# Kernel tuning notes

Hardware: AMD Instinct MI355X
Metric: run time of the kernel (lower is better)

Reference implementation:

```python
import jax, jax.numpy as jnp
import numpy as np

N, B, PG, L, HC, EC, H, NC, KNN = 256, 4, 64, 32, 128, 64, 4, 14, 8
D = HC // H
CUTOFF = 10.0
LOG2 = 0.6931471805599453

_counts = np.array([14, 5, 11, 8, 8, 6, 9, 9, 4, 10, 8, 8, 9, 8, 11, 7, 6, 7, 14, 12, 7])
RES_ATOM_MASK = (np.arange(14)[None, :] < _counts[:, None]).astype(np.float32)  # [21,14]


def _ln(x, g, b):
    mu = jnp.mean(x, -1, keepdims=True)
    var = jnp.mean((x - mu) ** 2, -1, keepdims=True)
    return (x - mu) / jnp.sqrt(var + 1e-5) * g + b


def _ssp(x):
    return jax.nn.softplus(x) - LOG2


def _safe_norm(x):
    return jnp.sqrt(jnp.maximum(jnp.sum(x * x, -1), 1e-12))


def _seg_softmax(x, idx, n):
    m = jax.ops.segment_max(x, idx, num_segments=n)
    e = jnp.exp(x - m[idx])
    s = jax.ops.segment_sum(e, idx, num_segments=n)
    return e / s[idx]


def _smear(d):
    offs = jnp.linspace(0.0, CUTOFF, EC)
    coeff = -0.5 / (offs[1] - offs[0]) ** 2
    return jnp.exp(coeff * (d[..., None] - offs) ** 2)


def _core(res_H, res_X, ligand_pos, ligand_feat, ligand_mask,
          ln_g, ln_b, ln1_g, ln1_b,
          WQ, WK, WV, WKl, WVl, WO, WOl, WOl1,
          Ti_w1, Ti_b1, Ti_w2, Ti_b2,
          sD_w1, sD_b1, sD_w2, sD_b2,
          sD1_w1, sD1_b1, sD1_w2, sD1_b2,
          res_S, batch, residue_mask, row1, col1):
    n = res_H.shape[0]
    bsz = ligand_feat.shape[0]
    lc = ligand_feat.shape[1]
    amask = jnp.asarray(RES_ATOM_MASK)[res_S]  # [n,14]

    # kNN graph on C-alpha (atom 1), per-graph, flow target_to_source, + self loops
    ctr = res_X[:, 1]
    d2 = jnp.sum((ctr[:, None] - ctr[None]) ** 2, -1)
    bad = (batch[:, None] != batch[None]) | jnp.eye(n, dtype=bool)
    _, nbr = jax.lax.top_k(-jnp.where(bad, jnp.inf, d2), KNN)
    row = jnp.concatenate([jnp.repeat(jnp.arange(n), KNN), jnp.arange(n)])
    col = jnp.concatenate([nbr.reshape(-1), jnp.arange(n)])

    Rij = _safe_norm(res_X[row][:, :, None] - res_X[col][:, None])  # [E,14,14]
    drep = _smear(Rij)  # [E,14,14,EC]

    res_Hn = _ln(res_H, ln_g, ln_b)
    Q = (res_Hn @ WQ.T).reshape(n, NC, H, D)
    Kt = (res_Hn @ WK.T).reshape(n, NC, H, D)
    V = (res_Hn @ WV.T).reshape(n, NC, H, D)

    logits = jnp.einsum('ephd,eqhd->ehpq', Q[row], Kt[col]) / np.sqrt(D)
    sig = jax.nn.relu(drep @ sD_w1.T + sD_b1) @ sD_w2.T + sD_b2  # [E,14,14,H]
    logits = logits + sig.transpose(0, 3, 1, 2)

    am_e = amask[row][:, :, None] * amask[col][:, None]  # [E,14,14]
    r = jnp.einsum('ep,ehpq,eq->eh', amask[row], logits, amask[col])
    r = r / jnp.sum(am_e, (-1, -2))[:, None]
    beta = _seg_softmax(r, row, n)  # [E,H]

    att = jax.nn.softmax(logits, -1) * am_e[:, None]
    att = att / (jnp.sum(jnp.abs(att), -1, keepdims=True) + 1e-7)
    aV = jnp.einsum('ehpq,eqhd->ehpd', att, V[col])
    updH = jax.ops.segment_sum(beta[:, :, None, None] * aV, row, num_segments=n)
    updH = updH.transpose(0, 2, 1, 3).reshape(n, NC, HC)
    res_H2 = (res_Hn + _ssp(updH) @ WO.T) * amask[..., None]

    Xij = res_X[row][:, :, None] - res_X[col][:, None]  # [E,14,14,3]
    Xij = Xij / (_safe_norm(Xij)[..., None] + 1e-5)
    Qf = Q.reshape(n, NC, HC)
    Kf = Kt.reshape(n, NC, HC)
    # T_i on concat([Q_p, K_q, dist]) computed as split matmuls (no big concat)
    hmid = (Qf[row] @ Ti_w1[:, :HC].T)[:, :, None, :] \
        + (Kf[col] @ Ti_w1[:, HC:2 * HC].T)[:, None, :, :] \
        + drep @ Ti_w1[:, 2 * HC:].T + Ti_b1  # [E,14,14,HC]
    f = (jax.nn.relu(hmid) @ Ti_w2.T + Ti_b2)[..., 0]  # [E,14,14]
    f = f * jnp.mean(att, 1)
    dX = jax.ops.segment_sum(jnp.mean(beta, -1)[:, None, None]
                             * jnp.sum(f[..., None] * Xij, -2), row, num_segments=n)
    res_X2 = jnp.where(residue_mask[:, None, None],
                       res_X + jnp.clip(dX, -3.0, 3.0), res_X)

    # residue <-> ligand cross attention over (editable residue, graph) edges
    lf = _ln(ligand_feat, ln1_g, ln1_b)
    Kl = (lf @ WKl.T).reshape(bsz, lc, H, D)
    Vl = (lf @ WVl.T).reshape(bsz, lc, H, D)
    Rij1 = _safe_norm(res_X2[row1][:, :, None] - ligand_pos[col1][:, None])
    drep1 = _smear(Rij1)  # [E1,14,L,EC]
    lg = jnp.einsum('ephd,eqhd->ehpq', Q[row1], Kl[col1]) / np.sqrt(D)
    sig1 = jax.nn.relu(drep1 @ sD1_w1.T + sD1_b1) @ sD1_w2.T + sD1_b2
    lg = lg + sig1.transpose(0, 3, 1, 2)

    am1 = amask[row1][:, :, None] * ligand_mask[col1][:, None]  # [E1,14,L]
    r1 = jnp.einsum('ep,ehpq,eq->eh', amask[row1], lg, ligand_mask[col1])
    r1 = r1 / jnp.sum(am1, (-1, -2))[:, None]
    beta1 = _seg_softmax(r1, col1, bsz)

    ar = jax.nn.softmax(lg, -1) * am1[:, None]
    ar = ar / (jnp.sum(jnp.abs(ar), -1, keepdims=True) + 1e-7)
    al = jax.nn.softmax(lg, -2) * am1[:, None]
    # faithful to source: lig branch divided by L1 norm of already-normalized ar
    al = al / (jnp.sum(jnp.abs(ar), -1, keepdims=True) + 1e-7)
    aVr = jnp.einsum('ehpq,eqhd->ehpd', ar, Vl[col1])  # [E1,H,14,D]
    e1 = row1.shape[0]
    res_H3 = res_H2.at[row1].add(
        _ssp(aVr.transpose(0, 2, 1, 3).reshape(e1, NC, HC)) @ WOl.T)
    res_H3 = res_H3 * amask[..., None]
    aVlg = jnp.einsum('ehpq,ephd->ehqd', al, V[row1])  # [E1,H,L,D]
    updL = jax.ops.segment_sum(beta1[:, :, None, None] * aVlg, col1, num_segments=bsz)
    lf2 = lf + _ssp(updL.transpose(0, 2, 1, 3).reshape(bsz, lc, HC)) @ WOl1.T
    return res_H3, res_X2, lf2


def setup_inputs() -> dict:
    key = jax.random.key(0)
    ks = jax.random.split(key, 40)
    rn = lambda i, shape, s=1.0: jax.random.normal(ks[i], shape, jnp.float32) * s
    w = lambda i, shape: jax.random.normal(ks[i], shape, jnp.float32) * 0.05
    res_H = rn(0, (N, NC, HC))
    res_X = rn(1, (N, NC, 3), 4.0)
    res_S = jax.random.randint(ks[2], (N,), 0, 21)
    batch = jnp.repeat(jnp.arange(B), PG)
    residue_mask = (jnp.arange(N) % PG) < 16
    row1 = jnp.asarray(np.nonzero(np.asarray(residue_mask))[0])
    col1 = row1 // PG
    ligand_pos = rn(3, (B, L, 3), 4.0)
    ligand_feat = rn(4, (B, L, HC))
    ligand_mask = jnp.tile((jnp.arange(L) < 24).astype(jnp.float32)[None], (B, 1))
    return dict(
        res_H=res_H, res_X=res_X, ligand_pos=ligand_pos, ligand_feat=ligand_feat,
        ligand_mask=ligand_mask,
        ln_g=jnp.ones((HC,)), ln_b=jnp.zeros((HC,)),
        ln1_g=jnp.ones((HC,)), ln1_b=jnp.zeros((HC,)),
        WQ=w(5, (HC, HC)), WK=w(6, (HC, HC)), WV=w(7, (HC, HC)),
        WKl=w(8, (HC, HC)), WVl=w(9, (HC, HC)),
        WO=w(10, (HC, HC)), WOl=w(11, (HC, HC)), WOl1=w(12, (HC, HC)),
        Ti_w1=w(13, (HC, 2 * HC + EC)), Ti_b1=jnp.zeros((HC,)),
        Ti_w2=w(14, (1, HC)), Ti_b2=jnp.zeros((1,)),
        sD_w1=w(15, (HC, EC)), sD_b1=jnp.zeros((HC,)),
        sD_w2=w(16, (H, HC)), sD_b2=jnp.zeros((H,)),
        sD1_w1=w(17, (HC, EC)), sD1_b1=jnp.zeros((HC,)),
        sD1_w2=w(18, (H, HC)), sD1_b2=jnp.zeros((H,)),
        res_S=res_S, batch=batch, residue_mask=residue_mask, row1=row1, col1=col1)


def reference(res_H, res_X, ligand_pos, ligand_feat, ligand_mask,
              ln_g, ln_b, ln1_g, ln1_b,
              WQ, WK, WV, WKl, WVl, WO, WOl, WOl1,
              Ti_w1, Ti_b1, Ti_w2, Ti_b2,
              sD_w1, sD_b1, sD_w2, sD_b2,
              sD1_w1, sD1_b1, sD1_w2, sD1_b2,
              res_S, batch, residue_mask, row1, col1):
    return _core(res_H, res_X, ligand_pos, ligand_feat, ligand_mask,
                 ln_g, ln_b, ln1_g, ln1_b,
                 WQ, WK, WV, WKl, WVl, WO, WOl, WOl1,
                 Ti_w1, Ti_b1, Ti_w2, Ti_b2,
                 sD_w1, sD_b1, sD_w2, sD_b2,
                 sD1_w1, sD1_b1, sD1_w2, sD1_b2,
                 res_S, batch, residue_mask, row1, col1)
```

## Files before the change

kernel.cpp:

```cpp
#include <hip/hip_runtime.h>
#include <hip/hip_bf16.h>
#include <math.h>

typedef __hip_bfloat16 bf16;

#define NRES 256
#define LC   32
#define HCH  128
#define ECH  64
#define NH   4
#define NCA  14
#define KNNK 8
#define DH   32
#define NKE  (NRES*KNNK)
#define NEDGE (NKE+NRES)
#define NE1  64
#define NROWS (NRES*NCA)

#define NT     3073
#define TSCALE 256.0f
#define DMAXT  12.0f

#define O_RESH   0
#define O_RESX   458752
#define O_LPOS   469504
#define O_LFEAT  469888
#define O_LMASK  486272
#define O_LNG    486400
#define O_LNB    486528
#define O_LN1G   486656
#define O_LN1B   486784
#define O_WQ     486912
#define O_WK     503296
#define O_WV     519680
#define O_WKL    536064
#define O_WVL    552448
#define O_WO     568832
#define O_WOL    585216
#define O_WOL1   601600
#define O_TIW1   617984
#define O_TIB1   658944
#define O_TIW2   659072
#define O_TIB2   659200
#define O_SDW1   659204
#define O_SDB1   667396
#define O_SDW2   667524
#define O_SDB2   668036
#define O_SD1W1  668040
#define O_SD1B1  676232
#define O_SD1W2  676360
#define O_SD1B2  676872
#define TOTCVT   676876
#define CVT_RSV  676880

#define OUTX_OFF 458752
#define OUTL_OFF 469504

__constant__ int c_counts[21] = {14,5,11,8,8,6,9,9,4,10,8,8,9,8,11,7,6,7,14,12,7};

using bfrag = __attribute__((ext_vector_type(8))) short;
using f32x4 = __attribute__((ext_vector_type(4))) float;

__device__ __forceinline__ float b2f(bf16 x){ return __bfloat162float(x); }
__device__ __forceinline__ float sspf(float x){
  return fmaxf(x,0.f) + log1pf(expf(-fabsf(x))) - 0.6931471805599453f;
}
__device__ __forceinline__ float bflo(unsigned u){ return __uint_as_float(u<<16); }
__device__ __forceinline__ float bfhi(unsigned u){ return __uint_as_float(u & 0xffff0000u); }
__device__ __forceinline__ unsigned short f2bs(float v){ bf16 b=__float2bfloat16(v); return *(unsigned short*)&b; }
__device__ __forceinline__ unsigned pack2(float a, float b){
  return (unsigned)f2bs(a) | ((unsigned)f2bs(b)<<16);
}
__device__ __forceinline__ int ccount(int s){ return c_counts[s<0?0:(s>20?20:s)]; }
__device__ __forceinline__ void storeOut(void* out, int isbf, int idx, float v){
  if (isbf) ((bf16*)out)[idx] = __float2bfloat16(v);
  else      ((float*)out)[idx] = v;
}

__global__ __launch_bounds__(256) void kcvt(
    const void* s0,const void* s1,const void* s2,const void* s3,const void* s4,
    const void* s5,const void* s6,const void* s7,const void* s8,const void* s9,
    const void* s10,const void* s11,const void* s12,const void* s13,const void* s14,
    const void* s15,const void* s16,const void* s17,const void* s18,const void* s19,
    const void* s20,const void* s21,const void* s22,const void* s23,const void* s24,
    const void* s25,const void* s26,const void* s27,const void* s28,
    float* __restrict__ dst, int* __restrict__ flag)
{
  __shared__ int sflag;
  int tid = threadIdx.x;
  if (tid < 64){
    unsigned w = ((const unsigned*)s0)[tid];
    unsigned lo = w & 0xFFFFu;
    int ee = (lo >> 7) & 0xFF;
    int good = (lo == 0u) || (ee >= 121 && ee <= 133);
    unsigned long long m = __ballot(good);
    if (tid == 0){
      sflag = (__popcll(m) >= 40) ? 1 : 0;
      if (blockIdx.x == 0) flag[0] = sflag;
    }
  }
  __syncthreads();
  int isbf = sflag;
  int g = blockIdx.x*256 + tid;
  if (g >= TOTCVT) return;
  const void* src; int l;
  if      (g < O_RESX ) { src=s0;  l=g; }
  else if (g < O_LPOS ) { src=s1;  l=g-O_RESX; }
  else if (g < O_LFEAT) { src=s2;  l=g-O_LPOS; }
  else if (g < O_LMASK) { src=s3;  l=g-O_LFEAT; }
  else if (g < O_LNG  ) { src=s4;  l=g-O_LMASK; }
  else if (g < O_LNB  ) { src=s5;  l=g-O_LNG; }
  else if (g < O_LN1G ) { src=s6;  l=g-O_LNB; }
  else if (g < O_LN1B ) { src=s7;  l=g-O_LN1G; }
  else if (g < O_WQ   ) { src=s8;  l=g-O_LN1B; }
  else if (g < O_WK   ) { src=s9;  l=g-O_WQ; }
  else if (g < O_WV   ) { src=s10; l=g-O_WK; }
  else if (g < O_WKL  ) { src=s11; l=g-O_WV; }
  else if (g < O_WVL  ) { src=s12; l=g-O_WKL; }
  else if (g < O_WO   ) { src=s13; l=g-O_WVL; }
  else if (g < O_WOL  ) { src=s14; l=g-O_WO; }
  else if (g < O_WOL1 ) { src=s15; l=g-O_WOL; }
  else if (g < O_TIW1 ) { src=s16; l=g-O_WOL1; }
  else if (g < O_TIB1 ) { src=s17; l=g-O_TIW1; }
  else if (g < O_TIW2 ) { src=s18; l=g-O_TIB1; }
  else if (g < O_TIB2 ) { src=s19; l=g-O_TIW2; }
  else if (g < O_SDW1 ) { src=s20; l=0; }
  else if (g < O_SDB1 ) { src=s21; l=g-O_SDW1; }
  else if (g < O_SDW2 ) { src=s22; l=g-O_SDB1; }
  else if (g < O_SDB2 ) { src=s23; l=g-O_SDW2; }
  else if (g < O_SD1W1) { src=s24; l=g-O_SDB2; }
  else if (g < O_SD1B1) { src=s25; l=g-O_SD1W1; }
  else if (g < O_SD1W2) { src=s26; l=g-O_SD1B1; }
  else if (g < O_SD1B2) { src=s27; l=g-O_SD1W2; }
  else                  { src=s28; l=g-O_SD1B2; }
  float v = isbf ? b2f(((const bf16*)src)[l]) : ((const float*)src)[l];
  dst[g] = v;
}

__global__ __launch_bounds__(128) void kprep(const float* __restrict__ cvt, const int* __restrict__ row1,
    unsigned* __restrict__ ctab, float* __restrict__ sig1T,
    float* __restrict__ wt, int* __restrict__ inv_row)
{
  int b = blockIdx.x, o = threadIdx.x;
  if (b >= NT){
    int cb = b - NT;
    if (cb < 1280){
      int gid = cb*128 + o;
      int m = gid >> 14;
      int j = gid & 16383;
      int oo = j >> 7, c = j & 127;
      float v;
      switch(m){
        case 0: v = cvt[O_WQ  + j]; break;
        case 1: v = cvt[O_WK  + j]; break;
        case 2: v = cvt[O_WV  + j]; break;
        case 3: v = cvt[O_WO  + j]; break;
        case 4: v = cvt[O_WKL + j]; break;
        case 5: v = cvt[O_WVL + j]; break;
        case 6: v = cvt[O_WOL + j]; break;
        case 7: v = cvt[O_WOL1+ j]; break;
        case 8: v = cvt[O_TIW1 + oo*320 + c]; break;
        default:v = cvt[O_TIW1 + oo*320 + 128 + c]; break;
      }
      wt[m*16384 + c*128 + oo] = v;
    } else {
      for (int i=o;i<NRES;i+=128) inv_row[i] = -1;
      __syncthreads();
      if (o < NE1) inv_row[row1[o] & 255] = o;
    }
    return;
  }
  __shared__ float dr[64];
  __shared__ float W[128*65];
  __shared__ float h1[128], h1b[128];
  __shared__ float sgb[4];
  float d = (float)b * (1.0f/256.0f);
  const float step = 10.0f/63.0f;
  const float coef = -0.5f/(step*step);
  if (o < 64){ float t = d - step*(float)o; dr[o] = expf(coef*t*t); }
  for (int idx=o; idx<8192; idx+=128){ int oo=idx>>6, k=idx&63; W[oo*65+k] = cvt[O_TIW1 + oo*320 + 256 + k]; }
  __syncthreads();
  {
    float c = cvt[O_TIB1+o];
    for (int k=0;k<64;k++) c += dr[k]*W[o*65+k];
    float cn = __shfl_xor(c, 1);
    if (!(o&1)) ctab[(size_t)b*68 + 2 + (o>>1)] = pack2(c, cn);
  }
  __syncthreads();
  for (int idx=o; idx<8192; idx+=128){ int oo=idx>>6, k=idx&63; W[oo*65+k] = cvt[O_SDW1 + idx]; }
  __syncthreads();
  {
    float a = cvt[O_SDB1+o];
    for (int k=0;k<64;k++) a += dr[k]*W[o*65+k];
    h1[o] = fmaxf(a,0.f);
  }
  __syncthreads();
  for (int idx=o; idx<8192; idx+=128){ int oo=idx>>6, k=idx&63; W[oo*65+k] = cvt[O_SD1W1 + idx]; }
  __syncthreads();
  {
    float a2 = cvt[O_SD1B1+o];
    for (int k=0;k<64;k++) a2 += dr[k]*W[o*65+k];
    h1b[o] = fmaxf(a2,0.f);
  }
  __syncthreads();
  if (o < 8){
    int h = o & 3;
    const float* hh = (o<4)? h1 : h1b;
    int wbase = (o<4)? O_SDW2 : O_SD1W2;
    int bbase = (o<4)? O_SDB2 : O_SD1B2;
    float s = cvt[bbase + h];
    for (int k=0;k<128;k++) s += hh[k]*cvt[wbase + h*128 + k];
    if (o<4) sgb[h] = s; else sig1T[b*4+h] = s;
  }
  __syncthreads();
  if (o==0) ctab[(size_t)b*68 + 0] = pack2(sgb[0], sgb[1]);
  else if (o==1) ctab[(size_t)b*68 + 1] = pack2(sgb[2], sgb[3]);
  else if (o==2) ctab[(size_t)b*68 + 66] = 0u;
  else if (o==3) ctab[(size_t)b*68 + 67] = 0u;
}

__global__ __launch_bounds__(256) void kProjAll(
    const float* __restrict__ cvt, const float* __restrict__ wt, const int* __restrict__ batch,
    float* __restrict__ resHn, bf16* __restrict__ Qw16, bf16* __restrict__ Kw16,
    bf16* __restrict__ Vw16, bf16* __restrict__ TQw16, bf16* __restrict__ TKw16,
    int* __restrict__ nbr, float* __restrict__ lf, bf16* __restrict__ Klw16, bf16* __restrict__ Vlw16)
{
  __shared__ float Xs[16*129];
  __shared__ float x2[2][HCH];
  __shared__ float sred2[2][2];
  int bb = blockIdx.x, tid = threadIdx.x;

  if (bb < 672){
    int m = bb / 224;
    int rt = (bb % 224) * 16;
    for (int i=tid; i<16*128; i+=256){
      int r=i>>7, c=i&127;
      Xs[r*129+c] = cvt[O_RESH + (rt+r)*HCH + c];
    }
    __syncthreads();
    {
      int wave = tid>>6, lane = tid&63;
      int r = wave*4 + (lane>>4);
      int cb = lane & 15;
      float s=0;
      #pragma unroll
      for (int j=0;j<8;j++) s += Xs[r*129 + cb + 16*j];
      #pragma unroll
      for (int off=1; off<16; off<<=1) s += __shfl_xor(s, off);
      float mu = s*(1.f/HCH);
      float q=0;
      #pragma unroll
      for (int j=0;j<8;j++){ float dv = Xs[r*129+cb+16*j]-mu; q += dv*dv; }
      #pragma unroll
      for (int off=1; off<16; off<<=1) q += __shfl_xor(q, off);
      float inv = rsqrtf(q*(1.f/HCH) + 1e-5f);
      #pragma unroll
      for (int j=0;j<8;j++){
        int c = cb + 16*j;
        float xh = (Xs[r*129+c]-mu)*inv*cvt[O_LNG+c] + cvt[O_LNB+c];
        Xs[r*129+c] = xh;
        if (m==0) resHn[(rt+r)*HCH+c] = xh;
      }
    }
    __syncthreads();
    int tc = (tid & 31) * 4;
    int tr = (tid >> 5) * 2;
    const float* W = wt + m*16384;
    float a00=0,a01=0,a02=0,a03=0, a10=0,a11=0,a12=0,a13=0;
    for (int c=0;c<HCH;c++){
      float4 w4 = *(const float4*)(W + c*128 + tc);
      float x0 = Xs[tr*129 + c];
      float x1 = Xs[(tr+1)*129 + c];
      a00 += x0*w4.x; a01 += x0*w4.y; a02 += x0*w4.z; a03 += x0*w4.w;
      a10 += x1*w4.x; a11 += x1*w4.y; a12 += x1*w4.z; a13 += x1*w4.w;
    }
    bf16* out = (m==0)? Qw16 : (m==1)? Kw16 : Vw16;
    {
      unsigned* o0 = (unsigned*)(out + (rt+tr  )*HCH + tc);
      unsigned* o1 = (unsigned*)(out + (rt+tr+1)*HCH + tc);
      o0[0]=pack2(a00,a01); o0[1]=pack2(a02,a03);
      o1[0]=pack2(a10,a11); o1[1]=pack2(a12,a13);
    }
    if (m == 2) return;
    __syncthreads();
    Xs[tr*129+tc]=a00; Xs[tr*129+tc+1]=a01; Xs[tr*129+tc+2]=a02; Xs[tr*129+tc+3]=a03;
    Xs[(tr+1)*129+tc]=a10; Xs[(tr+1)*129+tc+1]=a11; Xs[(tr+1)*129+tc+2]=a12; Xs[(tr+1)*129+tc+3]=a13;
    __syncthreads();
    const float* W2 = wt + (8+m)*16384;
    a00=0;a01=0;a02=0;a03=0; a10=0;a11=0;a12=0;a13=0;
    for (int c=0;c<HCH;c++){
      float4 w4 = *(const float4*)(W2 + c*128 + tc);
      float x0 = Xs[tr*129 + c];
      float x1 = Xs[(tr+1)*129 + c];
      a00 += x0*w4.x; a01 += x0*w4.y; a02 += x0*w4.z; a03 += x0*w4.w;
      a10 += x1*w4.x; a11 += x1*w4.y; a12 += x1*w4.z; a13 += x1*w4.w;
    }
    bf16* out2 = m ? TKw16 : TQw16;
    {
      unsigned* o0 = (unsigned*)(out2 + (rt+tr  )*HCH + tc);
      unsigned* o1 = (unsigned*)(out2 + (rt+tr+1)*HCH + tc);
      o0[0]=pack2(a00,a01); o0[1]=pack2(a02,a03);
      o1[0]=pack2(a10,a11); o1[1]=pack2(a12,a13);
    }
    return;
  }

  if (bb < 736){
    int wave = tid>>6, lane = tid&63;
    int n = (bb-672)*4 + wave;
    float cx = cvt[O_RESX+(n*NCA+1)*3+0];
    float cy = cvt[O_RESX+(n*NCA+1)*3+1];
    float cz = cvt[O_RESX+(n*NCA+1)*3+2];
    int bn = batch[n];
    float d2v[4]; int idv[4];
    #pragma unroll
    for (int t=0;t<4;t++){
      int j = lane + 64*t;
      float jx = cvt[O_RESX+(j*NCA+1)*3+0];
      float jy = cvt[O_RESX+(j*NCA+1)*3+1];
      float jz = cvt[O_RESX+(j*NCA+1)*3+2];
      float dx=cx-jx, dy=cy-jy, dz=cz-jz;
      float d2 = dx*dx+dy*dy+dz*dz;
      bool bad = (batch[j]!=bn) || (j==n);
      d2v[t] = bad ? INFINITY : d2;
      idv[t] = j;
    }
    for (int k=0;k<KNNK;k++){
      float dm = d2v[0]; int im = idv[0];
      #pragma unroll
      for (int t=1;t<4;t++)
        if (d2v[t]<dm || (d2v[t]==dm && idv[t]<im)){ dm=d2v[t]; im=idv[t]; }
      #pragma unroll
      for (int off=1; off<64; off<<=1){
        float dn = __shfl_xor(dm, off);
        int   in = __shfl_xor(im, off);
        if (dn<dm || (dn==dm && in<im)){ dm=dn; im=in; }
      }
      if (lane==0) nbr[n*KNNK+k] = im;
      #pragma unroll
      for (int t=0;t<4;t++) if (idv[t]==im) d2v[t] = INFINITY;
    }
    return;
  }

  int row = tid>>7, t = tid&127;
  int rb = (bb-736)*2 + row;
  float v = cvt[O_LFEAT + rb*HCH + t];
  float s=v;
  for (int off=1; off<64; off<<=1) s += __shfl_xor(s, off);
  if ((t&63)==0) sred2[row][t>>6]=s;
  __syncthreads();
  float mu=(sred2[row][0]+sred2[row][1])*(1.f/HCH);
  __syncthreads();
  float d=v-mu; s=d*d;
  for (int off=1; off<64; off<<=1) s += __shfl_xor(s, off);
  if ((t&63)==0) sred2[row][t>>6]=s;
  __syncthreads();
  float var=(sred2[row][0]+sred2[row][1])*(1.f/HCH);
  float xh = d*rsqrtf(var+1e-5f)*cvt[O_LN1G+t] + cvt[O_LN1B+t];
  x2[row][t]=xh; lf[rb*HCH+t]=xh;
  __syncthreads();
  const float* WKlt = wt + 4*16384;
  const float* WVlt = wt + 5*16384;
  float aK=0.f, aV=0.f;
  for (int c=0;c<HCH;c++){
    float xc=x2[row][c];
    aK += xc*WKlt[c*128+t];
    aV += xc*WVlt[c*128+t];
  }
  Klw16[rb*HCH+t]=__float2bfloat16(aK);
  Vlw16[rb*HCH+t]=__float2bfloat16(aV);
}

#define PR1(cbu, tau, kau, wl, wh) \
  fa += fmaxf(bflo(tau)+bflo(kau)+bflo(cbu),0.f)*(wl) + fmaxf(bfhi(tau)+bfhi(kau)+bfhi(cbu),0.f)*(wh);

__global__ __launch_bounds__(256) void k3_edge(
    const float* __restrict__ cvt, const int* __restrict__ res_S, const int* __restrict__ nbr,
    const bf16* __restrict__ Qw16, const bf16* __restrict__ Kw16,
    const bf16* __restrict__ TQw16, const bf16* __restrict__ TKw16,
    const bf16* __restrict__ Vw16, const unsigned* __restrict__ ctab,
    float* __restrict__ r_ws, bf16* __restrict__ aVe16, float* __restrict__ dXe)
{
  __shared__ __align__(16) unsigned char UB[8192];
  __shared__ unsigned Tqp[14*66], Tkp[14*66];
  __shared__ float LG[4*16*17];
  __shared__ float FR[196];
  __shared__ __align__(16) float tw2s[132];
  __shared__ float tb2s[1], Xr[42], Xc[42], amr[14], amc[14], rpart[56], cnts[2];
  unsigned char* QbB = UB;
  unsigned char* KbB = UB + 4096;
  unsigned char* VtB = UB;

  int b = blockIdx.x, tid = threadIdx.x;
  int rr = b & 255, slot = b >> 8;
  int e  = (slot < 8) ? (rr*8 + slot) : (2048 + rr);
  int cc = (slot < 8) ? (nbr[rr*8 + slot] & 255) : rr;

  const unsigned* TQ32 = (const unsigned*)TQw16;
  const unsigned* TK32 = (const unsigned*)TKw16;

  {
    int row = tid >> 4, s16 = tid & 15;
    uint4 qv = {0u,0u,0u,0u}, kv = {0u,0u,0u,0u};
    if (row < 14){
      qv = ((const uint4*)(Qw16 + (size_t)rr*1792))[tid];
      kv = ((const uint4*)(Kw16 + (size_t)cc*1792))[tid];
    }
    int off = row*256 + ((s16 ^ (row & 7)) << 4);
    *(uint4*)(QbB + off) = qv;
    *(uint4*)(KbB + off) = kv;
  }
  for (int i = tid; i < 14*66; i += 256){
    int p = i/66, t = i - p*66;
    Tqp[i] = (t<64) ? TQ32[rr*896 + p*64 + t] : 0u;
    Tkp[i] = (t<64) ? TK32[cc*896 + p*64 + t] : 0u;
  }
  if (tid < 132) tw2s[tid] = (tid<128) ? cvt[O_TIW2+tid] : 0.f;
  if (tid == 132) tb2s[0] = cvt[O_TIB2];
  if (tid >= 136 && tid < 178){
    int i=tid-136; int p=i/3, jx=i%3;
    Xr[i] = cvt[O_RESX+(rr*NCA+p)*3+jx];
    Xc[i] = cvt[O_RESX+(cc*NCA+p)*3+jx];
  }
  if (tid >= 242 && tid < 242+NCA){
    int p=tid-242;
    amr[p] = (p < ccount(res_S[rr])) ? 1.f : 0.f;
    amc[p] = (p < ccount(res_S[cc])) ? 1.f : 0.f;
  }
  __syncthreads();

  {
    int w = tid >> 6, l = tid & 63;
    int mrow = l & 15, s = l >> 4;
    int aoff = mrow*256 + (((w*4 + s) ^ (mrow & 7)) << 4);
    bfrag a = *(const bfrag*)(QbB + aoff);
    bfrag bkf = *(const bfrag*)(KbB + aoff);
    f32x4 dacc = {0.f,0.f,0.f,0.f};
    dacc = __builtin_amdgcn_mfma_f32_16x16x32_bf16(a, bkf, dacc, 0, 0, 0);
    const float isq = 0.17677669529663687f;
    #pragma unroll
    for (int r=0;r<4;r++){
      int p = s*4 + r;
      LG[w*272 + p*17 + mrow] = dacc[r]*isq;
    }
  }

  float sgx=0.f, sgy=0.f, sgz=0.f, sgw=0.f, invd_r=0.f;
  int havePair = (tid < 196);
  if (havePair){
    int p = tid/14, q = tid%14;
    float dx=Xr[p*3]-Xc[q*3], dy=Xr[p*3+1]-Xc[q*3+1], dz=Xr[p*3+2]-Xc[q*3+2];
    float d = sqrtf(fmaxf(dx*dx+dy*dy+dz*dz, 1e-12f));
    invd_r = 1.f/(d + 1e-5f);
    int i0 = (int)(fminf(d, DMAXT)*TSCALE + 0.5f);
    const uint4* crow = (const uint4*)ctab + (size_t)i0*17;
    const unsigned* TqpRow = Tqp + p*66;
    const unsigned* TkpRow = Tkp + q*66;
    uint4 h0 = crow[0];
    sgx = bflo(h0.x); sgy = bfhi(h0.x); sgz = bflo(h0.y); sgw = bfhi(h0.y);
    float fa = tb2s[0];
    {
      uint2 ta = *(const uint2*)(TqpRow);
      uint2 ka = *(const uint2*)(TkpRow);
      float4 w0 = *(const float4*)(tw2s);
      PR1(h0.z, ta.x, ka.x, w0.x, w0.y);
      PR1(h0.w, ta.y, ka.y, w0.z, w0.w);
    }
    #pragma unroll 4
    for (int j=1;j<17;j++){
      uint4 ch = crow[j];
      int t = 4*j - 2;
      uint2 ta0 = *(const uint2*)(TqpRow + t);
      uint2 ta1 = *(const uint2*)(TqpRow + t + 2);
      uint2 ka0 = *(const uint2*)(TkpRow + t);
      uint2 ka1 = *(const uint2*)(TkpRow + t + 2);
      float4 w0 = *(const float4*)(tw2s + 2*t);
      float4 w1 = *(const float4*)(tw2s + 2*t + 4);
      PR1(ch.x, ta0.x, ka0.x, w0.x, w0.y);
      PR1(ch.y, ta0.y, ka0.y, w0.z, w0.w);
      PR1(ch.z, ta1.x, ka1.x, w1.x, w1.y);
      PR1(ch.w, ta1.y, ka1.y, w1.z, w1.w);
    }
    FR[tid] = fa;
  }
  __syncthreads();

  if (havePair){
    int p = tid/14, q = tid%14;
    LG[      p*17+q] += sgx;
    LG[272 + p*17+q] += sgy;
    LG[544 + p*17+q] += sgz;
    LG[816 + p*17+q] += sgw;
  }
  for (int i = tid; i < 128*16; i += 256){
    int qp = i >> 7, d = i & 127;
    int qq = qp*2;
    unsigned pv = 0u;
    if (qq < 14){
      const unsigned short* vs = (const unsigned short*)(Vw16 + (size_t)cc*1792);
      unsigned short v0 = vs[qq*128 + d];
      unsigned short v1 = vs[(qq+1)*128 + d];
      pv = (unsigned)v0 | ((unsigned)v1 << 16);
    }
    int slotq = qq >> 3;
    int off = d*64 + ((slotq ^ (d & 3)) << 4) + (qq & 7)*2;
    *(unsigned*)(VtB + off) = pv;
  }
  __syncthreads();

  if (tid < 56){
    int h=tid/14, pp=tid%14;
    float ap = amr[pp];
    float* rowp = LG + h*272 + pp*17;
    float row[NCA];
    float s=0;
    #pragma unroll
    for (int qq=0;qq<NCA;qq++){ row[qq]=rowp[qq]; s += row[qq]*amc[qq]; }
    rpart[h*14+pp] = s*ap;
    float m=-INFINITY;
    #pragma unroll
    for (int qq=0;qq<NCA;qq++) m=fmaxf(m,row[qq]);
    float sum=0;
    #pragma unroll
    for (int qq=0;qq<NCA;qq++){ row[qq]=expf(row[qq]-m); sum+=row[qq]; }
    float inv=1.f/sum, s2=0;
    #pragma unroll
    for (int qq=0;qq<NCA;qq++){ row[qq]=row[qq]*inv*ap*amc[qq]; s2+=row[qq]; }
    float inv2=1.f/(s2+1e-7f);
    #pragma unroll
    for (int qq=0;qq<NCA;qq++) rowp[qq]=row[qq]*inv2;
  }
  if (tid == 56){
    float sr=0, sc=0;
    for (int i=0;i<NCA;i++){ sr+=amr[i]; sc+=amc[i]; }
    cnts[0]=sr; cnts[1]=sc;
  }
  __syncthreads();
  if (tid < NH){
    float s=0;
    for (int pp=0;pp<NCA;pp++) s += rpart[tid*14+pp];
    r_ws[e*NH+tid] = s/(cnts[0]*cnts[1]);
  }
  if (tid < 196){
    int p=tid/14, q=tid%14;
    float ma = 0.25f*(LG[p*17+q] + LG[272+p*17+q] + LG[544+p*17+q] + LG[816+p*17+q]);
    FR[tid] *= ma * invd_r;
  }

  {
    int w = tid >> 6, l = tid & 63;
    int mrow = l & 15, s = l >> 4;
    bfrag pa;
    if (s < 2){
      const float* ar = LG + w*272 + mrow*17 + s*8;
      #pragma unroll
      for (int j=0;j<8;j++) pa[j] = (short)f2bs(ar[j]);
    } else {
      #pragma unroll
      for (int j=0;j<8;j++) pa[j] = (short)0;
    }
    #pragma unroll
    for (int half=0; half<2; half++){
      int dg = w*32 + half*16 + mrow;
      int boff = dg*64 + ((s ^ (dg & 3)) << 4);
      bfrag pb = *(const bfrag*)(VtB + boff);
      f32x4 dd = {0.f,0.f,0.f,0.f};
      dd = __builtin_amdgcn_mfma_f32_16x16x32_bf16(pa, pb, dd, 0, 0, 0);
      #pragma unroll
      for (int r=0;r<4;r++){
        int p = s*4 + r;
        if (p < NCA)
          aVe16[(size_t)e*1792 + w*448 + p*32 + half*16 + mrow] = __float2bfloat16(dd[r]);
      }
    }
  }
  __syncthreads();

  if (tid < NCA*3){
    int pp = tid/3, jx = tid%3;
    float a=0;
    #pragma unroll
    for (int qq=0;qq<NCA;qq++){
      float diff = Xr[pp*3+jx]-Xc[qq*3+jx];
      a += FR[pp*14+qq]*diff;
    }
    dXe[(e*NCA+pp)*3+jx] = a;
  }
}

__global__ __launch_bounds__(256) void k4_agg(
    const float* __restrict__ cvt, const int* __restrict__ res_S, const int* __restrict__ inv_row,
    const float* __restrict__ r_ws, const bf16* __restrict__ aVe16, const float* __restrict__ dXe,
    const float* __restrict__ resHn, const float* __restrict__ wt, const int* __restrict__ flag,
    float* __restrict__ resH2, float* __restrict__ resX2, void* __restrict__ d_out)
{
  int n = blockIdx.x, tid = threadIdx.x;
  __shared__ float beta[9][NH];
  __shared__ float betam[9];
  __shared__ float Xs[NCA][HCH];
  if (tid < NH){
    int h = tid;
    float rv[9], m=-INFINITY;
    #pragma unroll
    for (int k=0;k<9;k++){
      int ek = (k<KNNK)? n*KNNK+k : NKE+n;
      rv[k] = r_ws[ek*NH+h];
      m = fmaxf(m, rv[k]);
    }
    float s=0;
    #pragma unroll
    for (int k=0;k<9;k++){ rv[k]=expf(rv[k]-m); s+=rv[k]; }
    #pragma unroll
    for (int k=0;k<9;k++) beta[k][h]=rv[k]/s;
  }
  __syncthreads();
  if (tid < 9) betam[tid] = 0.25f*(beta[tid][0]+beta[tid][1]+beta[tid][2]+beta[tid][3]);
  int col = tid & 127, ph = tid >> 7;
  int h = col>>5, dd = col&31;
  float bh[9];
  #pragma unroll
  for (int k=0;k<9;k++) bh[k]=beta[k][h];
  #pragma unroll
  for (int i=0;i<7;i++){
    int p = ph + 2*i;
    float u=0;
    #pragma unroll
    for (int k=0;k<9;k++){
      int ek = (k<KNNK)? n*KNNK+k : NKE+n;
      u += bh[k]*b2f(aVe16[ek*1792 + h*448 + p*32 + dd]);
    }
    Xs[p][col] = sspf(u);
  }
  __syncthreads();
  const float* WOt = wt + 3*16384;
  float acc[7];
  #pragma unroll
  for (int i=0;i<7;i++) acc[i]=0.f;
  for (int c=0;c<HCH;c++){
    float w = WOt[c*128+col];
    #pragma unroll
    for (int i=0;i<7;i++) acc[i] += Xs[ph+2*i][c]*w;
  }
  int cnt = ccount(res_S[n]);
  #pragma unroll
  for (int i=0;i<7;i++){
    int p = ph + 2*i;
    float am = (p<cnt)?1.f:0.f;
    float outv = (resHn[(n*NCA+p)*HCH+col] + acc[i])*am;
    resH2[(n*NCA+p)*HCH+col] = outv;
  }
  if (tid < NCA*3){
    int isbf = *flag;
    int p=tid/3, jx=tid%3;
    float s=0;
    #pragma unroll
    for (int k=0;k<9;k++){
      int ek=(k<KNNK)? n*KNNK+k : NKE+n;
      s += betam[k]*dXe[(ek*NCA+p)*3+jx];
    }
    float base = cvt[O_RESX+(n*NCA+p)*3+jx];
    float v = (inv_row[n]>=0) ? base + fminf(fmaxf(s,-3.f),3.f) : base;
    resX2[(n*NCA+p)*3+jx] = v;
    storeOut(d_out, isbf, OUTX_OFF + (n*NCA+p)*3+jx, v);
  }
}

__global__ __launch_bounds__(256) void k6_lig(
    const float* __restrict__ cvt, const int* __restrict__ res_S,
    const int* __restrict__ row1, const int* __restrict__ col1,
    const float* __restrict__ resX2, const bf16* __restrict__ Qw16, const bf16* __restrict__ Klw16,
    const bf16* __restrict__ Vw16, const bf16* __restrict__ Vlw16, const float* __restrict__ sig1T,
    float* __restrict__ r1_ws, float* __restrict__ aVr, float* __restrict__ aVlg)
{
  __shared__ float Bq[14*33], Vrs[14*33], Bk[32*33], Vls[32*33];
  __shared__ float LG[14*33], ALs[14*33];
  __shared__ float Xr[42], Lp[96], amr[14], lm[32], s2r[14], rpart[14], cnts[2];
  int bb = blockIdx.x, tid = threadIdx.x;
  int e = bb >> 2, h = bb & 3;
  int rr = row1[e] & 255, cb = col1[e] & 3;
  const unsigned* Q32  = (const unsigned*)Qw16;
  const unsigned* V32  = (const unsigned*)Vw16;
  const unsigned* Kl32 = (const unsigned*)Klw16;
  const unsigned* Vl32 = (const unsigned*)Vlw16;

  for (int i=tid; i<224; i+=256){
    int p=i>>4, dp=i&15;
    unsigned q2 = Q32[rr*896 + p*64 + h*16 + dp];
    unsigned v2 = V32[rr*896 + p*64 + h*16 + dp];
    Bq[p*33+2*dp]  = bflo(q2); Bq[p*33+2*dp+1]  = bfhi(q2);
    Vrs[p*33+2*dp] = bflo(v2); Vrs[p*33+2*dp+1] = bfhi(v2);
  }
  for (int i=tid; i<512; i+=256){
    int q=i>>4, dp=i&15;
    unsigned k2 = Kl32[cb*2048 + q*64 + h*16 + dp];
    unsigned w2 = Vl32[cb*2048 + q*64 + h*16 + dp];
    Bk[q*33+2*dp]  = bflo(k2); Bk[q*33+2*dp+1]  = bfhi(k2);
    Vls[q*33+2*dp] = bflo(w2); Vls[q*33+2*dp+1] = bfhi(w2);
  }
  if (tid >= 8 && tid < 50){ int i=tid-8; int p=i/3,jx=i%3; Xr[i]=resX2[(rr*NCA+p)*3+jx]; }
  if (tid >= 64 && tid < 160){ int i=tid-64; Lp[i]=cvt[O_LPOS + cb*96 + i]; }
  if (tid >= 160 && tid < 174) amr[tid-160]=((tid-160) < ccount(res_S[rr]))?1.f:0.f;
  if (tid >= 192 && tid < 224) lm[tid-192]=cvt[O_LMASK + cb*LC + tid-192];
  __syncthreads();

  const float isq=0.17677669529663687f;
  for (int pair=tid; pair<448; pair+=256){
    int p=pair>>5, q=pair&31;
    float dx=Xr[p*3]-Lp[q*3], dy=Xr[p*3+1]-Lp[q*3+1], dz=Xr[p*3+2]-Lp[q*3+2];
    float d=sqrtf(fmaxf(dx*dx+dy*dy+dz*dz,1e-12f));
    int i0=(int)(fminf(d,DMAXT)*TSCALE+0.5f);
    float sg = sig1T[i0*4+h];
    float qk=0;
    #pragma unroll
    for (int dd=0;dd<DH;dd++) qk += Bq[p*33+dd]*Bk[q*33+dd];
    LG[p*33+q] = qk*isq + sg;
  }
  __syncthreads();

  if (tid < 14){
    int pp=tid; float ap=amr[pp];
    float s=0, m=-INFINITY;
    for (int qq=0;qq<LC;qq++){ float v=LG[pp*33+qq]; s+=v*lm[qq]; m=fmaxf(m,v); }
    rpart[pp]=s*ap;
    float sum=0;
    for (int qq=0;qq<LC;qq++) sum+=expf(LG[pp*33+qq]-m);
    float inv=1.f/sum, s2=0;
    for (int qq=0;qq<LC;qq++) s2+=expf(LG[pp*33+qq]-m)*inv*ap*lm[qq];
    s2r[pp]=s2/(s2+1e-7f);
  }
  if (tid==14){ float sr=0; for(int i=0;i<14;i++) sr+=amr[i]; cnts[0]=sr; }
  if (tid==15){ float sl=0; for(int i=0;i<32;i++) sl+=lm[i]; cnts[1]=sl; }
  __syncthreads();

  if (tid==0){ float s=0; for (int pp=0;pp<14;pp++) s+=rpart[pp]; r1_ws[e*NH+h]=s/(cnts[0]*cnts[1]); }
  if (tid < 32){
    int qq=tid;
    float m=-INFINITY;
    for (int pp=0;pp<14;pp++) m=fmaxf(m,LG[pp*33+qq]);
    float sum=0;
    for (int pp=0;pp<14;pp++) sum+=expf(LG[pp*33+qq]-m);
    float inv=1.f/sum, lq=lm[qq];
    for (int pp=0;pp<14;pp++){
      float a=expf(LG[pp*33+qq]-m)*inv*amr[pp]*lq;
      ALs[pp*33+qq]=a/(s2r[pp]+1e-7f);
    }
  }
  __syncthreads();

  if (tid < 14){
    int pp=tid; float ap=amr[pp];
    float m=-INFINITY;
    for (int qq=0;qq<LC;qq++) m=fmaxf(m,LG[pp*33+qq]);
    float row[LC]; float sum=0;
    for (int qq=0;qq<LC;qq++){ row[qq]=expf(LG[pp*33+qq]-m); sum+=row[qq]; }
    float inv=1.f/sum, s2=0;
    for (int qq=0;qq<LC;qq++){ row[qq]=row[qq]*inv*ap*lm[qq]; s2+=row[qq]; }
    float inv2=1.f/(s2+1e-7f);
    for (int qq=0;qq<LC;qq++) LG[pp*33+qq]=row[qq]*inv2;
  }
  __syncthreads();

  for (int j=tid;j<448;j+=256){
    int pp=j>>5, dd=j&31;
    float acc=0;
    #pragma unroll
    for (int qq=0;qq<LC;qq++) acc += LG[pp*33+qq]*Vls[qq*33+dd];
    aVr[e*1792 + h*448 + j]=acc;
  }
  for (int j=tid;j<1024;j+=256){
    int qq=j>>5, dd=j&31;
    float acc=0;
    #pragma unroll
    for (int pp=0;pp<14;pp++) acc += ALs[pp*33+qq]*Vrs[pp*33+dd];
    aVlg[e*4096 + h*1024 + j]=acc;
  }
}

__global__ __launch_bounds__(256) void k78_final(
    const int* __restrict__ inv_row, const int* __restrict__ res_S, const int* __restrict__ col1,
    const float* __restrict__ resH2, const float* __restrict__ aVr,
    const float* __restrict__ r1_ws, const float* __restrict__ aVlg, const float* __restrict__ lf,
    const float* __restrict__ wt, const int* __restrict__ flag, void* __restrict__ d_out)
{
  int bb = blockIdx.x, tid = threadIdx.x;
  if (bb < 256){
    int n = bb;
    int e = inv_row[n];
    __shared__ float G[NCA][HCH];
    if (e>=0){
      for (int j=tid;j<NCA*HCH;j+=256){
        int h=j/448, rem=j%448, pp=rem>>5, dd=rem&31;
        G[pp][h*DH+dd] = sspf(aVr[e*1792+j]);
      }
    }
    __syncthreads();
    int col = tid & 127, ph = tid >> 7;
    float acc[7];
    #pragma unroll
    for (int i=0;i<7;i++) acc[i]=0.f;
    if (e>=0){
      const float* WOlt = wt + 6*16384;
      for (int c=0;c<HCH;c++){
        float w=WOlt[c*128+col];
        #pragma unroll
        for (int i=0;i<7;i++) acc[i]+=G[ph+2*i][c]*w;
      }
    }
    int cnt=ccount(res_S[n]);
    int isbf = *flag;
    #pragma unroll
    for (int i=0;i<7;i++){
      int p = ph + 2*i;
      float am=(p<cnt)?1.f:0.f;
      float v=(resH2[(n*NCA+p)*HCH+col]+acc[i])*am;
      storeOut(d_out, isbf, (n*NCA+p)*HCH+col, v);
    }
    return;
  }
  int rb = bb - 256;
  int b = rb>>5, q = rb&31;
  __shared__ float bw[NE1][NH];
  __shared__ float xs[HCH];
  if (tid<NH){
    int h=tid;
    float m=-INFINITY;
    for (int e=0;e<NE1;e++) if ((col1[e]&3)==b) m=fmaxf(m, r1_ws[e*NH+h]);
    float s=0;
    for (int e=0;e<NE1;e++) if ((col1[e]&3)==b) s+=expf(r1_ws[e*NH+h]-m);
    for (int e=0;e<NE1;e++) bw[e][h] = ((col1[e]&3)==b)? expf(r1_ws[e*NH+h]-m)/s : 0.f;
  }
  __syncthreads();
  if (tid < 128){
    int h=tid>>5, dd=tid&31;
    float u=0;
    for (int e=0;e<NE1;e++) u += bw[e][h]*aVlg[e*4096 + h*1024 + q*32 + dd];
    xs[tid]=sspf(u);
  }
  __syncthreads();
  if (tid < 128){
    const float* WOl1t = wt + 7*16384;
    float acc=0;
    for (int c=0;c<HCH;c++) acc += xs[c]*WOl1t[c*128+tid];
    float v = lf[rb*HCH+tid] + acc;
    storeOut(d_out, *flag, OUTL_OFF + rb*HCH+tid, v);
  }
}

extern "C" void kernel_launch(void* const* d_in, const int* in_sizes, int n_in,
                              void* d_out, int out_size, void* d_ws, size_t ws_size,
                              hipStream_t stream)
{
  const int* res_S = (const int*)d_in[29];
  const int* batch = (const int*)d_in[30];
  const int* row1  = (const int*)d_in[32];
  const int* col1  = (const int*)d_in[33];

  float* wsf = (float*)d_ws;
  size_t o = 0;
  int*   flag    = (int*)(wsf + o); o += 4;
  float* cvt     = wsf + o; o += CVT_RSV;
  float* wt      = wsf + o; o += 10*16384;
  int*   inv_row = (int*)(wsf + o); o += 256;
  int*   nbr     = (int*)(wsf + o); o += NRES*KNNK;
  float* resHn   = wsf + o; o += NROWS*HCH;
  bf16*  Qw16    = (bf16*)(wsf + o); o += NROWS*HCH/2;
  bf16*  Kw16    = (bf16*)(wsf + o); o += NROWS*HCH/2;
  bf16*  Vw16    = (bf16*)(wsf + o); o += NROWS*HCH/2;
  bf16*  TQw16   = (bf16*)(wsf + o); o += NROWS*HCH/2;
  bf16*  TKw16   = (bf16*)(wsf + o); o += NROWS*HCH/2;
  float* r_ws    = wsf + o; o += NEDGE*NH;
  bf16*  aVe16   = (bf16*)(wsf + o); o += (size_t)NEDGE*1792/2;
  float* dXe     = wsf + o; o += NEDGE*NCA*3;
  float* resH2   = wsf + o; o += NROWS*HCH;
  float* resX2   = wsf + o; o += NRES*NCA*3;
  float* lf      = wsf + o; o += 4*LC*HCH;
  bf16*  Klw16   = (bf16*)(wsf + o); o += 4*LC*HCH/2;
  bf16*  Vlw16   = (bf16*)(wsf + o); o += 4*LC*HCH/2;
  float* r1w     = wsf + o; o += NE1*NH;
  float* aVrw    = wsf + o; o += NE1*1792;
  float* aVlgw   = wsf + o; o += NE1*4096;
  unsigned* ctab = (unsigned*)(wsf + o); o += (size_t)NT*68;
  float* sig1T   = wsf + o; o += NT*4;

  kcvt<<<(TOTCVT+255)/256, 256, 0, stream>>>(
      d_in[0],d_in[1],d_in[2],d_in[3],d_in[4],d_in[5],d_in[6],d_in[7],d_in[8],
      d_in[9],d_in[10],d_in[11],d_in[12],d_in[13],d_in[14],d_in[15],d_in[16],
      d_in[17],d_in[18],d_in[19],d_in[20],d_in[21],d_in[22],d_in[23],d_in[24],
      d_in[25],d_in[26],d_in[27],d_in[28], cvt, flag);
  kprep<<<NT + 1280 + 1, 128, 0, stream>>>(cvt, row1, ctab, sig1T, wt, inv_row);
  kProjAll<<<800, 256, 0, stream>>>(cvt, wt, batch, resHn, Qw16, Kw16, Vw16, TQw16, TKw16,
                                    nbr, lf, Klw16, Vlw16);
  k3_edge<<<NEDGE, 256, 0, stream>>>(cvt, res_S, nbr, Qw16, Kw16, TQw16, TKw16, Vw16, ctab,
                                     r_ws, aVe16, dXe);
  k4_agg<<<NRES, 256, 0, stream>>>(cvt, res_S, inv_row, r_ws, aVe16, dXe, resHn, wt, flag,
                                   resH2, resX2, d_out);
  k6_lig<<<NE1*NH, 256, 0, stream>>>(cvt, res_S, row1, col1, resX2, Qw16, Klw16, Vw16, Vlw16, sig1T,
                                     r1w, aVrw, aVlgw);
  k78_final<<<384, 256, 0, stream>>>(inv_row, res_S, col1, resH2, aVrw, r1w, aVlgw, lf,
                                     wt, flag, d_out);
}
```

Before: 264.9 us.

## Restructure distance-table precompute as tiled register-blocked GEMM over 32-row tiles

The per-distance lookup-table build used to run one block per table row (3073 blocks), and each block reloaded three 128x64 weight matrices into shared memory. It now runs 291 blocks, each covering a 32-row tile for one of the three MLPs. Each thread keeps 16 accumulators and loads the weights once per tile. The Gaussian smearing table is precomputed in the conversion kernel and written to global memory. This trades redundant weight reloads and synchronisation for a larger shared-memory footprint and an extra workspace buffer.

```diff
diff --git a/kernel.cpp b/kernel.cpp
--- a/kernel.cpp
+++ b/kernel.cpp
@@ -56,6 +56,10 @@
 #define OUTX_OFF 458752
 #define OUTL_OFF 469504
 
+#define CVB  ((TOTCVT+255)/256)
+#define NEB  ((NT*64+255)/256)
+#define NGEMM 291
+
 __constant__ int c_counts[21] = {14,5,11,8,8,6,9,9,4,10,8,8,9,8,11,7,6,7,14,12,7};
 
 using bfrag = __attribute__((ext_vector_type(8))) short;
@@ -84,10 +88,22 @@
     const void* s15,const void* s16,const void* s17,const void* s18,const void* s19,
     const void* s20,const void* s21,const void* s22,const void* s23,const void* s24,
     const void* s25,const void* s26,const void* s27,const void* s28,
-    float* __restrict__ dst, int* __restrict__ flag)
+    float* __restrict__ dst, int* __restrict__ flag, float* __restrict__ etab)
 {
+  int bb = blockIdx.x;
+  int tid = threadIdx.x;
+  if (bb >= CVB){
+    int idx = (bb - CVB)*256 + tid;
+    if (idx < NT*64){
+      int bq = idx >> 6, k = idx & 63;
+      const float step = 10.0f/63.0f;
+      const float coef = -0.5f/(step*step);
+      float t = (float)bq*(1.0f/256.0f) - step*(float)k;
+      etab[idx] = expf(coef*t*t);
+    }
+    return;
+  }
   __shared__ int sflag;
-  int tid = threadIdx.x;
   if (tid < 64){
     unsigned w = ((const unsigned*)s0)[tid];
     unsigned lo = w & 0xFFFFu;
@@ -101,7 +117,7 @@
   }
   __syncthreads();
   int isbf = sflag;
-  int g = blockIdx.x*256 + tid;
+  int g = bb*256 + tid;
   if (g >= TOTCVT) return;
   const void* src; int l;
   if      (g < O_RESX ) { src=s0;  l=g; }
@@ -137,15 +153,16 @@
   dst[g] = v;
 }
 
-__global__ __launch_bounds__(128) void kprep(const float* __restrict__ cvt, const int* __restrict__ row1,
+__global__ __launch_bounds__(256) void kprep(const float* __restrict__ cvt, const float* __restrict__ Etab,
+    const int* __restrict__ row1,
     unsigned* __restrict__ ctab, float* __restrict__ sig1T,
     float* __restrict__ wt, int* __restrict__ inv_row)
 {
-  int b = blockIdx.x, o = threadIdx.x;
-  if (b >= NT){
-    int cb = b - NT;
-    if (cb < 1280){
-      int gid = cb*128 + o;
+  int b = blockIdx.x, tid = threadIdx.x;
+  if (b >= NGEMM){
+    int cb = b - NGEMM;
+    if (cb < 640){
+      int gid = cb*256 + tid;
       int m = gid >> 14;
       int j = gid & 16383;
       int oo = j >> 7, c = j & 127;
@@ -164,59 +181,103 @@
       }
       wt[m*16384 + c*128 + oo] = v;
     } else {
-      for (int i=o;i<NRES;i+=128) inv_row[i] = -1;
+      inv_row[tid] = -1;
       __syncthreads();
-      if (o < NE1) inv_row[row1[o] & 255] = o;
+      if (tid < NE1) inv_row[row1[tid] & 255] = tid;
     }
     return;
   }
-  __shared__ float dr[64];
-  __shared__ float W[128*65];
-  __shared__ float h1[128], h1b[128];
-  __shared__ float sgb[4];
-  float d = (float)b * (1.0f/256.0f);
-  const float step = 10.0f/63.0f;
-  const float coef = -0.5f/(step*step);
-  if (o < 64){ float t = d - step*(float)o; dr[o] = expf(coef*t*t); }
-  for (int idx=o; idx<8192; idx+=128){ int oo=idx>>6, k=idx&63; W[oo*65+k] = cvt[O_TIW1 + oo*320 + 256 + k]; }
-  __syncthreads();
-  {
-    float c = cvt[O_TIB1+o];
-    for (int k=0;k<64;k++) c += dr[k]*W[o*65+k];
-    float cn = __shfl_xor(c, 1);
-    if (!(o&1)) ctab[(size_t)b*68 + 2 + (o>>1)] = pack2(c, cn);
-  }
-  __syncthreads();
-  for (int idx=o; idx<8192; idx+=128){ int oo=idx>>6, k=idx&63; W[oo*65+k] = cvt[O_SDW1 + idx]; }
-  __syncthreads();
-  {
-    float a = cvt[O_SDB1+o];
-    for (int k=0;k<64;k++) a += dr[k]*W[o*65+k];
-    h1[o] = fmaxf(a,0.f);
-  }
-  __syncthreads();
-  for (int idx=o; idx<8192; idx+=128){ int oo=idx>>6, k=idx&63; W[oo*65+k] = cvt[O_SD1W1 + idx]; }
-  __syncthreads();
-  {
-    float a2 = cvt[O_SD1B1+o];
-    for (int k=0;k<64;k++) a2 += dr[k]*W[o*65+k];
-    h1b[o] = fmaxf(a2,0.f);
-  }
-  __syncthreads();
-  if (o < 8){
-    int h = o & 3;
-    const float* hh = (o<4)? h1 : h1b;
-    int wbase = (o<4)? O_SDW2 : O_SD1W2;
-    int bbase = (o<4)? O_SDB2 : O_SD1B2;
-    float s = cvt[bbase + h];
-    for (int k=0;k<128;k++) s += hh[k]*cvt[wbase + h*128 + k];
-    if (o<4) sgb[h] = s; else sig1T[b*4+h] = s;
-  }
-  __syncthreads();
-  if (o==0) ctab[(size_t)b*68 + 0] = pack2(sgb[0], sgb[1]);
-  else if (o==1) ctab[(size_t)b*68 + 1] = pack2(sgb[2], sgb[3]);
-  else if (o==2) ctab[(size_t)b*68 + 66] = 0u;
-  else if (o==3) ctab[(size_t)b*68 + 67] = 0u;
+  __shared__ float Wl[128*68];
+  __shared__ float Et[32*68];
+  __shared__ float H[32*132];
+  __shared__ float W2[4*132];
+  __shared__ float W2b[4];
+  int mt = b % 97, m = b / 97;
+  int r0 = mt*32;
+  int nr = (NT - r0 < 32) ? (NT - r0) : 32;
+
+  for (int idx=tid; idx<8192; idx+=256){
+    int o=idx>>6, k=idx&63;
+    float v = (m==0) ? cvt[O_TIW1 + o*320 + 256 + k]
+            : (m==1) ? cvt[O_SDW1 + idx]
+                     : cvt[O_SD1W1 + idx];
+    Wl[o*68+k] = v;
+  }
+  for (int idx=tid; idx<nr*64; idx+=256){
+    int r=idx>>6, k=idx&63;
+    Et[r*68+k] = Etab[(size_t)(r0+r)*64 + k];
+  }
+  if (m >= 1){
+    int wbase = (m==1)? O_SDW2 : O_SD1W2;
+    int bbase = (m==1)? O_SDB2 : O_SD1B2;
+    for (int idx=tid; idx<512; idx+=256)
+      W2[(idx>>7)*132 + (idx&127)] = cvt[wbase + idx];
+    if (tid < 4) W2b[tid] = cvt[bbase + tid];
+  }
+  __syncthreads();
+
+  int o = tid & 127, g = tid >> 7;
+  int boff = (m==0)? O_TIB1 : (m==1)? O_SDB1 : O_SD1B1;
+  float bias = cvt[boff + o];
+  float acc[16];
+  #pragma unroll
+  for (int i=0;i<16;i++) acc[i] = bias;
+  const float* wrow = Wl + o*68;
+  const float* ebase = Et + g*16*68;
+  for (int kc=0; kc<16; kc++){
+    float4 w4 = *(const float4*)(wrow + kc*4);
+    #pragma unroll
+    for (int i=0;i<16;i++){
+      float4 e4 = *(const float4*)(ebase + i*68 + kc*4);
+      acc[i] += e4.x*w4.x;
+      acc[i] += e4.y*w4.y;
+      acc[i] += e4.z*w4.z;
+      acc[i] += e4.w*w4.w;
+    }
+  }
+
+  if (m == 0){
+    #pragma unroll
+    for (int i=0;i<16;i++){
+      int row = r0 + g*16 + i;
+      float c = acc[i];
+      float cn = __shfl_xor(c, 1);
+      if (row < NT && !(o&1))
+        ctab[(size_t)row*68 + 2 + (o>>1)] = pack2(c, cn);
+    }
+    if (o < 2 && g == 0){
+      for (int i=0;i<32;i++){
+        int row = r0 + i;
+        if (row < NT) ctab[(size_t)row*68 + 66 + o] = 0u;
+      }
+    }
+    return;
+  }
+  #pragma unroll
+  for (int i=0;i<16;i++)
+    H[(g*16+i)*132 + o] = fmaxf(acc[i], 0.f);
+  __syncthreads();
+  if (tid < 128){
+    int r = tid >> 2, hh = tid & 3;
+    int row = r0 + r;
+    if (r < nr){
+      float s = W2b[hh];
+      const float* hr = H + r*132;
+      const float* w2r = W2 + hh*132;
+      for (int o2=0;o2<128;o2++) s += hr[o2]*w2r[o2];
+      if (m == 1){
+        float s1 = __shfl_down(s,1);
+        float s2 = __shfl_down(s,2);
+        float s3 = __shfl_down(s,3);
+        if (hh == 0){
+          ctab[(size_t)row*68 + 0] = pack2(s, s1);
+          ctab[(size_t)row*68 + 1] = pack2(s2, s3);
+        }
+      } else {
+        sig1T[row*4 + hh] = s;
+      }
+    }
+  }
 }
 
 __global__ __launch_bounds__(256) void kProjAll(
@@ -882,13 +943,14 @@
   float* aVlgw   = wsf + o; o += NE1*4096;
   unsigned* ctab = (unsigned*)(wsf + o); o += (size_t)NT*68;
   float* sig1T   = wsf + o; o += NT*4;
-
-  kcvt<<<(TOTCVT+255)/256, 256, 0, stream>>>(
+  float* Etab    = wsf + o; o += (size_t)NT*64;
+
+  kcvt<<<CVB + NEB, 256, 0, stream>>>(
       d_in[0],d_in[1],d_in[2],d_in[3],d_in[4],d_in[5],d_in[6],d_in[7],d_in[8],
       d_in[9],d_in[10],d_in[11],d_in[12],d_in[13],d_in[14],d_in[15],d_in[16],
       d_in[17],d_in[18],d_in[19],d_in[20],d_in[21],d_in[22],d_in[23],d_in[24],
-      d_in[25],d_in[26],d_in[27],d_in[28], cvt, flag);
-  kprep<<<NT + 1280 + 1, 128, 0, stream>>>(cvt, row1, ctab, sig1T, wt, inv_row);
+      d_in[25],d_in[26],d_in[27],d_in[28], cvt, flag, Etab);
+  kprep<<<NGEMM + 640 + 1, 256, 0, stream>>>(cvt, Etab, row1, ctab, sig1T, wt, inv_row);
   kProjAll<<<800, 256, 0, stream>>>(cvt, wt, batch, resHn, Qw16, Kw16, Vw16, TQw16, TKw16,
                                     nbr, lf, Klw16, Vlw16);
   k3_edge<<<NEDGE, 256, 0, stream>>>(cvt, res_S, nbr, Qw16, Kw16, TQw16, TKw16, Vw16, ctab,
```

After: 236.3 us. 1.12x faster.
